# Kernel tuning notes

Measured on AMD Instinct MI355X. Metric: run time of the kernel, lower is better.

## Reference

```python
import jax, jax.numpy as jnp
import numpy as np

TEMPERATURE = 0.5

def setup_inputs() -> dict:
    key = jax.random.key(0)
    k1, k2 = jax.random.split(key)
    z_i = jax.random.normal(k1, (4096, 128), dtype=jnp.float32)
    z_j = jax.random.normal(k2, (4096, 128), dtype=jnp.float32)
    return {"z_i": z_i, "z_j": z_j}

def reference(z_i, z_j):
    n = z_i.shape[0]
    # L2 normalize each view (eps matches torch F.normalize default 1e-12)
    def l2norm(x):
        return x / jnp.maximum(jnp.linalg.norm(x, axis=1, keepdims=True), 1e-12)
    z = jnp.concatenate([l2norm(z_i), l2norm(z_j)], axis=0)  # [2N, D]
    sim = (z @ z.T) / TEMPERATURE                             # [2N, 2N]
    m = 2 * n
    idx = jnp.arange(m)
    pos_idx = jnp.concatenate([jnp.arange(n, m), jnp.arange(n)])  # positive pair index
    pos = sim[idx, pos_idx]                                   # [2N]
    # Per original: logits = [pos] ++ (row with diagonal removed); positive thus
    # appears twice in the logsumexp. Mask diagonal with -inf, prepend pos column.
    neg_inf = jnp.finfo(sim.dtype).min
    sim_masked = jnp.where(idx[:, None] == idx[None, :], neg_inf, sim)
    logits = jnp.concatenate([pos[:, None], sim_masked], axis=1)  # [2N, 2N+1]
    lse = jax.nn.logsumexp(logits, axis=1)
    loss = jnp.mean(lse - pos)
    return loss
```

## Files before the change

### kernel.cpp

```cpp
#include <hip/hip_runtime.h>
#include <hip/hip_bf16.h>

#define M_ROWS 8192
#define HALF_N 4096
#define D 128
#define NT 8
#define NCHUNK 8
#define E2C 2.8853900817779268f

typedef __attribute__((ext_vector_type(4))) float f32x4;
typedef __attribute__((ext_vector_type(8))) short bf16x8;
typedef unsigned int u32;
typedef __attribute__((ext_vector_type(4))) u32 u32x4;

__global__ __launch_bounds__(256) void k_normalize(
    const float* __restrict__ zi, const float* __restrict__ zj,
    __hip_bfloat16* __restrict__ zb)
{
    int t = blockIdx.x * 256 + threadIdx.x;
    int row  = t >> 6;
    int lane = t & 63;
    const float* src = (row < HALF_N) ? (zi + (size_t)row * D)
                                      : (zj + (size_t)(row - HALF_N) * D);
    float2 v = *(const float2*)(src + lane * 2);
    float ss = v.x * v.x + v.y * v.y;
    #pragma unroll
    for (int o = 32; o >= 1; o >>= 1) ss += __shfl_xor(ss, o);
    float scale = 1.0f / fmaxf(sqrtf(ss), 1e-12f);

    __hip_bfloat162 o2;
    o2.x = __float2bfloat16(v.x * scale);
    o2.y = __float2bfloat16(v.y * scale);
    *(__hip_bfloat162*)(zb + (size_t)row * D + lane * 2) = o2;
}

__global__ __launch_bounds__(256, 2) void k_simsum(
    const __hip_bfloat16* __restrict__ zb, float* __restrict__ rspart)
{
    __shared__ char sB[2][32768];

    const int chunk = blockIdx.x;
    const int pi    = blockIdx.y;
    const int ibase = pi * 128;
    const int jbase = chunk * (NT * 128);
    const int tid   = threadIdx.x;
    const int wv    = tid >> 6, lane = tid & 63;
    const int lr    = lane & 15, lg = lane >> 4;
    const int rbase = wv * 32;

    bf16x8 a[2][4];
    #pragma unroll
    for (int m = 0; m < 2; ++m)
        #pragma unroll
        for (int ks = 0; ks < 4; ++ks) {
            int row = ibase + rbase + m * 16 + lr;
            a[m][ks] = *(const bf16x8*)(zb + (size_t)row * D + (ks * 4 + lg) * 8);
        }

    u32x4 breg[8];
    auto load_tile = [&](int t) {
        const __hip_bfloat16* src = zb + (size_t)(jbase + t * 128) * D;
        #pragma unroll
        for (int i = 0; i < 8; ++i) {
            int row = (wv * 8 + i) * 4 + lg;
            breg[i] = *(const u32x4*)(src + (size_t)row * D + lr * 8);
        }
    };
    auto write_tile = [&](char* buf) {
        #pragma unroll
        for (int i = 0; i < 8; ++i) {
            int row = (wv * 8 + i) * 4 + lg;
            *(u32x4*)(buf + row * 256 + ((lr ^ (row & 7)) << 4)) = breg[i];
        }
    };

    float eacc[2][4] = {{0.f, 0.f, 0.f, 0.f}, {0.f, 0.f, 0.f, 0.f}};

    load_tile(0);
    write_tile(sB[0]);
    load_tile(1);
    __syncthreads();

    for (int t = 0; t < NT; ++t) {
        if (t + 1 < NT) write_tile(sB[(t + 1) & 1]);
        if (t + 2 < NT) load_tile(t + 2);

        const char* cur = sB[t & 1];
        f32x4 acc[2][8];
        #pragma unroll
        for (int m = 0; m < 2; ++m)
            #pragma unroll
            for (int n = 0; n < 8; ++n) acc[m][n] = (f32x4){0.f, 0.f, 0.f, 0.f};

        #pragma unroll
        for (int ks = 0; ks < 4; ++ks) {
            #pragma unroll
            for (int n = 0; n < 8; ++n) {
                int rowB = n * 16 + lr;
                bf16x8 bfr = *(const bf16x8*)(cur + rowB * 256 +
                              ((((ks << 2) + lg) ^ (lr & 7)) << 4));
                acc[0][n] = __builtin_amdgcn_mfma_f32_16x16x32_bf16(a[0][ks], bfr, acc[0][n], 0, 0, 0);
                acc[1][n] = __builtin_amdgcn_mfma_f32_16x16x32_bf16(a[1][ks], bfr, acc[1][n], 0, 0, 0);
            }
        }

        #pragma unroll
        for (int m = 0; m < 2; ++m)
            #pragma unroll
            for (int n = 0; n < 8; ++n)
                #pragma unroll
                for (int r = 0; r < 4; ++r)
                    eacc[m][r] += exp2f(acc[m][n][r] * E2C);

        __syncthreads();
    }

    #pragma unroll
    for (int m = 0; m < 2; ++m)
        #pragma unroll
        for (int r = 0; r < 4; ++r) {
            float e = eacc[m][r];
            e += __shfl_xor(e, 1);
            e += __shfl_xor(e, 2);
            e += __shfl_xor(e, 4);
            e += __shfl_xor(e, 8);
            if (lr == 0)
                rspart[chunk * M_ROWS + ibase + rbase + m * 16 + lg * 4 + r] = e;
        }
}

__global__ __launch_bounds__(256) void k_rowloss(
    const __hip_bfloat16* __restrict__ zb, const float* __restrict__ rspart,
    float* __restrict__ rowloss)
{
    int t = blockIdx.x * 256 + threadIdx.x;
    int row = t >> 6, lane = t & 63;
    int pair = row ^ HALF_N;

    float rs = (lane < NCHUNK) ? rspart[lane * M_ROWS + row] : 0.f;

    __hip_bfloat162 av = *(const __hip_bfloat162*)(zb + (size_t)row  * D + lane * 2);
    __hip_bfloat162 bv = *(const __hip_bfloat162*)(zb + (size_t)pair * D + lane * 2);
    float ax = __bfloat162float(av.x), ay = __bfloat162float(av.y);
    float bx = __bfloat162float(bv.x), by = __bfloat162float(bv.y);
    float sd = ax * ax + ay * ay;
    float pd = ax * bx + ay * by;
    #pragma unroll
    for (int o = 32; o >= 1; o >>= 1) {
        sd += __shfl_xor(sd, o);
        pd += __shfl_xor(pd, o);
        rs += __shfl_xor(rs, o);
    }
    if (lane == 0) {
        float val = rs - exp2f(sd * E2C) + exp2f(pd * E2C);
        rowloss[row] = logf(val) - 2.0f * pd;
    }
}

__global__ __launch_bounds__(1024) void k_reduce(
    const float* __restrict__ rowloss, float* __restrict__ out)
{
    __shared__ float sm[16];
    int tid = threadIdx.x;
    float s = 0.f;
    #pragma unroll
    for (int i = 0; i < M_ROWS / 1024; ++i) s += rowloss[i * 1024 + tid];
    #pragma unroll
    for (int o = 32; o >= 1; o >>= 1) s += __shfl_xor(s, o);
    if ((tid & 63) == 0) sm[tid >> 6] = s;
    __syncthreads();
    if (tid == 0) {
        float tot = 0.f;
        #pragma unroll
        for (int w = 0; w < 16; ++w) tot += sm[w];
        out[0] = tot * (1.0f / (float)M_ROWS);
    }
}

extern "C" void kernel_launch(void* const* d_in, const int* in_sizes, int n_in,
                              void* d_out, int out_size, void* d_ws, size_t ws_size,
                              hipStream_t stream)
{
    const float* zi = (const float*)d_in[0];
    const float* zj = (const float*)d_in[1];

    float* rspart  = (float*)d_ws;
    float* rowloss = (float*)((char*)d_ws + 262144);
    __hip_bfloat16* zb = (__hip_bfloat16*)((char*)d_ws + 262144 + 32768);

    k_normalize<<<dim3(M_ROWS * 64 / 256), 256, 0, stream>>>(zi, zj, zb);
    k_simsum<<<dim3(NCHUNK, 64), dim3(256), 0, stream>>>(zb, rspart);
    k_rowloss<<<dim3(M_ROWS * 64 / 256), 256, 0, stream>>>(zb, rspart, rowloss);
    k_reduce<<<dim3(1), dim3(1024), 0, stream>>>(rowloss, (float*)d_out);
}
```

Measured before the change: 45.05 us.

## Use 2x2 wave tiling, halve tiles per block, double grid in simsum

The per-wave tile in the similarity kernel changes from 32x128 to 64x64 by arranging the four waves in a 2x2 grid. This cuts LDS B-fragment reads per MFMA and raises register-level reuse. Each block now covers 4 column tiles instead of 8, giving a 16x64 grid (1024 blocks) for better CU occupancy. The prefetch pipeline is simplified to a single register tile with an extra barrier per iteration, and partial row sums grow to 32 slices that the row-loss kernel folds in. The cost is more partial sums and more accumulator and A registers per wave.

```diff
diff --git a/kernel.cpp b/kernel.cpp
--- a/kernel.cpp
+++ b/kernel.cpp
@@ -4,8 +4,8 @@
 #define M_ROWS 8192
 #define HALF_N 4096
 #define D 128
-#define NT 8
-#define NCHUNK 8
+#define NT 4
+#define NPART 32
 #define E2C 2.8853900817779268f
 
 typedef __attribute__((ext_vector_type(4))) float f32x4;
@@ -45,15 +45,15 @@
     const int jbase = chunk * (NT * 128);
     const int tid   = threadIdx.x;
     const int wv    = tid >> 6, lane = tid & 63;
+    const int wm    = wv >> 1,  wn   = wv & 1;
     const int lr    = lane & 15, lg = lane >> 4;
-    const int rbase = wv * 32;
-
-    bf16x8 a[2][4];
-    #pragma unroll
-    for (int m = 0; m < 2; ++m)
+
+    bf16x8 a[4][4];
+    #pragma unroll
+    for (int m = 0; m < 4; ++m)
         #pragma unroll
         for (int ks = 0; ks < 4; ++ks) {
-            int row = ibase + rbase + m * 16 + lr;
+            int row = ibase + wm * 64 + m * 16 + lr;
             a[m][ks] = *(const bf16x8*)(zb + (size_t)row * D + (ks * 4 + lg) * 8);
         }
 
@@ -74,49 +74,56 @@
         }
     };
 
-    float eacc[2][4] = {{0.f, 0.f, 0.f, 0.f}, {0.f, 0.f, 0.f, 0.f}};
+    float eacc[4][4];
+    #pragma unroll
+    for (int m = 0; m < 4; ++m)
+        #pragma unroll
+        for (int r = 0; r < 4; ++r) eacc[m][r] = 0.f;
 
     load_tile(0);
     write_tile(sB[0]);
-    load_tile(1);
     __syncthreads();
 
     for (int t = 0; t < NT; ++t) {
-        if (t + 1 < NT) write_tile(sB[(t + 1) & 1]);
-        if (t + 2 < NT) load_tile(t + 2);
-
+        if (t + 1 < NT) load_tile(t + 1);
         const char* cur = sB[t & 1];
-        f32x4 acc[2][8];
-        #pragma unroll
-        for (int m = 0; m < 2; ++m)
+
+        f32x4 acc[4][4];
+        #pragma unroll
+        for (int m = 0; m < 4; ++m)
             #pragma unroll
-            for (int n = 0; n < 8; ++n) acc[m][n] = (f32x4){0.f, 0.f, 0.f, 0.f};
+            for (int n = 0; n < 4; ++n) acc[m][n] = (f32x4){0.f, 0.f, 0.f, 0.f};
 
         #pragma unroll
         for (int ks = 0; ks < 4; ++ks) {
             #pragma unroll
-            for (int n = 0; n < 8; ++n) {
-                int rowB = n * 16 + lr;
+            for (int n = 0; n < 4; ++n) {
+                int rowB = wn * 64 + n * 16 + lr;
                 bf16x8 bfr = *(const bf16x8*)(cur + rowB * 256 +
                               ((((ks << 2) + lg) ^ (lr & 7)) << 4));
-                acc[0][n] = __builtin_amdgcn_mfma_f32_16x16x32_bf16(a[0][ks], bfr, acc[0][n], 0, 0, 0);
-                acc[1][n] = __builtin_amdgcn_mfma_f32_16x16x32_bf16(a[1][ks], bfr, acc[1][n], 0, 0, 0);
+                #pragma unroll
+                for (int m = 0; m < 4; ++m)
+                    acc[m][n] = __builtin_amdgcn_mfma_f32_16x16x32_bf16(a[m][ks], bfr, acc[m][n], 0, 0, 0);
             }
         }
 
         #pragma unroll
-        for (int m = 0; m < 2; ++m)
+        for (int m = 0; m < 4; ++m)
             #pragma unroll
-            for (int n = 0; n < 8; ++n)
+            for (int n = 0; n < 4; ++n)
                 #pragma unroll
                 for (int r = 0; r < 4; ++r)
                     eacc[m][r] += exp2f(acc[m][n][r] * E2C);
 
         __syncthreads();
-    }
-
-    #pragma unroll
-    for (int m = 0; m < 2; ++m)
+        if (t + 1 < NT) {
+            write_tile(sB[(t + 1) & 1]);
+            __syncthreads();
+        }
+    }
+
+    #pragma unroll
+    for (int m = 0; m < 4; ++m)
         #pragma unroll
         for (int r = 0; r < 4; ++r) {
             float e = eacc[m][r];
@@ -125,7 +132,8 @@
             e += __shfl_xor(e, 4);
             e += __shfl_xor(e, 8);
             if (lr == 0)
-                rspart[chunk * M_ROWS + ibase + rbase + m * 16 + lg * 4 + r] = e;
+                rspart[(chunk * 2 + wn) * M_ROWS +
+                       ibase + wm * 64 + m * 16 + lg * 4 + r] = e;
         }
 }
 
@@ -137,7 +145,7 @@
     int row = t >> 6, lane = t & 63;
     int pair = row ^ HALF_N;
 
-    float rs = (lane < NCHUNK) ? rspart[lane * M_ROWS + row] : 0.f;
+    float rs = (lane < NPART) ? rspart[lane * M_ROWS + row] : 0.f;
 
     __hip_bfloat162 av = *(const __hip_bfloat162*)(zb + (size_t)row  * D + lane * 2);
     __hip_bfloat162 bv = *(const __hip_bfloat162*)(zb + (size_t)pair * D + lane * 2);
@@ -185,11 +193,11 @@
     const float* zj = (const float*)d_in[1];
 
     float* rspart  = (float*)d_ws;
-    float* rowloss = (float*)((char*)d_ws + 262144);
-    __hip_bfloat16* zb = (__hip_bfloat16*)((char*)d_ws + 262144 + 32768);
+    float* rowloss = (float*)((char*)d_ws + 1048576);
+    __hip_bfloat16* zb = (__hip_bfloat16*)((char*)d_ws + 1048576 + 32768);
 
     k_normalize<<<dim3(M_ROWS * 64 / 256), 256, 0, stream>>>(zi, zj, zb);
-    k_simsum<<<dim3(NCHUNK, 64), dim3(256), 0, stream>>>(zb, rspart);
+    k_simsum<<<dim3(16, 64), dim3(256), 0, stream>>>(zb, rspart);
     k_rowloss<<<dim3(M_ROWS * 64 / 256), 256, 0, stream>>>(zb, rspart, rowloss);
     k_reduce<<<dim3(1), dim3(1024), 0, stream>>>(rowloss, (float*)d_out);
 }
```

New measurement: 59.65 us. 32.4% more time.
